# Kernel tuning notes

Measured on AMD Instinct MI355X. Metric: run time of the kernel, lower is better.

Reference implementation:

```python
import jax, jax.numpy as jnp
import numpy as np

N = 100000          # nodes
E = 1600000         # edges (avg degree 16)
D = 128             # prototype feature dim
C = 100             # num classes
NUM_LAYERS = 3      # propagation layers


def setup_inputs() -> dict:
    key = jax.random.key(0)
    k1, k2, k3, k4 = jax.random.split(key, 4)
    train_mask = jax.random.randint(k1, (N,), 0, 2) > 0                # bool [N]
    labels_all = jax.random.randint(k2, (N,), 0, C)                    # int   [N]
    edge_index = jax.random.randint(k3, (2, E), 0, N)                  # int   [2,E]
    global_protos = jax.random.normal(k4, (C, D), dtype=jnp.float32)   # [C,D]
    alpha = jnp.float32(0.5)                                           # learnable scalar
    return dict(train_mask=train_mask, global_protos=global_protos,
                labels_all=labels_all, edge_index=edge_index, alpha=alpha)


def _label_propagate(y0, edge_index, alpha):
    # symmetric GCN normalization D^-1/2 A D^-1/2 (no self loops), as in PyG LabelPropagation
    src, dst = edge_index[0], edge_index[1]
    deg = jax.ops.segment_sum(jnp.ones((E,), y0.dtype), dst, num_segments=N)
    deg_inv_sqrt = jnp.where(deg > 0, jax.lax.rsqrt(jnp.maximum(deg, 1.0)), 0.0)
    norm = deg_inv_sqrt[src] * deg_inv_sqrt[dst]                       # [E]
    res = (1.0 - alpha) * y0                                           # residual term
    out = y0
    for _ in range(NUM_LAYERS):
        msgs = out[src] * norm[:, None]                                # gather [E,D]
        agg = jax.ops.segment_sum(msgs, dst, num_segments=N)           # scatter-add [N,D]
        out = jnp.clip(alpha * agg + res, 0.0, 1.0)                    # post_step clamp
    return out


def reference(train_mask, global_protos, labels_all, edge_index, alpha):
    # proto_rep[train_mask] = global_protos[labels_all[train_mask]], zeros elsewhere
    y0 = jnp.where(train_mask[:, None], global_protos[labels_all], 0.0)  # [N,D]
    return _label_propagate(y0, edge_index, alpha)
```

## Files before the change

kernel.cpp:

```cpp
#include <hip/hip_runtime.h>
#include <stdint.h>

#define N_NODES 100000
#define N_EDGES 1600000
#define CAP     64
#define NBINS   1563
#define BINCAP  256
#define NSETS   8
#define CSTRIDE 16


__global__ void bin_kernel(const int* __restrict__ src, const int* __restrict__ dst,
                           int* __restrict__ cursor, unsigned int* __restrict__ bins) {
    int i = blockIdx.x * 256 + threadIdx.x;
    int set = blockIdx.x & 7;
    if (i < N_EDGES) {
        int s = src[i];
        int d = dst[i];
        int cid = set * NBINS + (d >> 6);
        int pos = atomicAdd(&cursor[cid * CSTRIDE], 1);
        if (pos < BINCAP)
            bins[(size_t)cid * BINCAP + pos] =
                (unsigned)s | ((unsigned)(d & 63) << 17);
    }
}


__global__ __launch_bounds__(256) void csr_kernel(
    const unsigned int* __restrict__ bins, const int* __restrict__ cursor,
    int* __restrict__ cnt, int* __restrict__ csr, float* __restrict__ dis,
    const int* __restrict__ mask, const int* __restrict__ labels,
    int* __restrict__ c0) {
    __shared__ int lc[64];
    int bin = blockIdx.x;
    int t = threadIdx.x;
    if (t < 64) lc[t] = 0;
    __syncthreads();
    int base = bin << 6;
    for (int set = 0; set < NSETS; ++set) {
        int cid = set * NBINS + bin;
        int m = cursor[cid * CSTRIDE];
        if (m > BINCAP) m = BINCAP;
        const unsigned int* seg = bins + (size_t)cid * BINCAP;
        for (int i = t; i < m; i += 256) {
            unsigned int v = seg[i];
            int dl = (int)(v >> 17);
            int pos = atomicAdd(&lc[dl], 1);
            if (pos < CAP) csr[(size_t)(base + dl) * CAP + pos] = (int)(v & 0x1FFFF);
        }
    }
    __syncthreads();
    if (t < 64) {
        int n = base + t;
        if (n < N_NODES) {
            int d = lc[t];
            cnt[n] = d;
            dis[n] = (d > 0) ? rsqrtf((float)d) : 0.0f;
            c0[n] = mask[n] ? labels[n] : -1;
        }
    }
}

template <int MODE>
__global__ __launch_bounds__(256) void prop_kernel(
    const uchar4* __restrict__ cur, void* __restrict__ out,
    const int* __restrict__ cnt, const int* __restrict__ csr,
    const float* __restrict__ dis, const int* __restrict__ c0,
    const float* __restrict__ protos, const float* __restrict__ alpha_p) {
    int wave = threadIdx.x >> 6;
    int lane = threadIdx.x & 63;
    int half = lane >> 5;
    int sub  = lane & 31;
    int base_lane = half << 5;
    int n = blockIdx.x * 8 + wave * 2 + half;

    float alpha = *alpha_p;
    int m = cnt[n];
    if (m > CAP) m = CAP;
    float dn = dis[n];
    const int* bucket = csr + (size_t)n * CAP;
    const float4* proto4 = (const float4*)protos;
    const float inv255 = 1.0f / 255.0f;

    int sl = 0;  float wl = 0.f;  int cl = -1;
    if (sub < m) {
        sl = bucket[sub];
        wl = dis[sl] * dn;
        if (MODE == 0) cl = c0[sl];
    }
    int sl2 = 0; float wl2 = 0.f; int cl2 = -1;
    if (m > 32 && 32 + sub < m) {
        sl2 = bucket[32 + sub];
        wl2 = dis[sl2] * dn;
        if (MODE == 0) cl2 = c0[sl2];
    }
    int m_other = __shfl(m, lane ^ 32);
    int mmax = m > m_other ? m : m_other;

    float a0 = 0.f, a1 = 0.f, a2 = 0.f, a3 = 0.f;

    if (MODE == 0) {
        for (int j = 0; j < mmax; j += 4) {
            float w[4]; float4 v[4];
            bool lo = j < 32;
#pragma unroll
            for (int k = 0; k < 4; ++k) {
                int e = j + k;
                float ww; int c;
                if (lo) { ww = __shfl(wl,  base_lane + e);      c = __shfl(cl,  base_lane + e); }
                else    { ww = __shfl(wl2, base_lane + e - 32); c = __shfl(cl2, base_lane + e - 32); }
                w[k] = ww;
                v[k] = (c >= 0) ? proto4[c * 32 + sub] : make_float4(0.f, 0.f, 0.f, 0.f);
            }
#pragma unroll
            for (int k = 0; k < 4; ++k) {
                a0 = fmaf(w[k], v[k].x, a0);
                a1 = fmaf(w[k], v[k].y, a1);
                a2 = fmaf(w[k], v[k].z, a2);
                a3 = fmaf(w[k], v[k].w, a3);
            }
        }
    } else {
        uchar4 u[8];  float w[8];
        uchar4 u2[8]; float w2[8];
#pragma unroll
        for (int k = 0; k < 8; ++k) {
            float ww = __shfl(wl, base_lane + k);
            int   s  = __shfl(sl, base_lane + k);
            w[k] = ww;
            u[k] = cur[(size_t)s * 32 + sub];
        }
        for (int j = 0; j < mmax; j += 8) {
            int jn = j + 8;
            if (jn < mmax) {
                bool lo = jn < 32;
#pragma unroll
                for (int k = 0; k < 8; ++k) {
                    int e = jn + k;
                    float ww; int s;
                    if (lo) { ww = __shfl(wl,  base_lane + e);      s = __shfl(sl,  base_lane + e); }
                    else    { ww = __shfl(wl2, base_lane + e - 32); s = __shfl(sl2, base_lane + e - 32); }
                    w2[k] = ww;
                    u2[k] = cur[(size_t)s * 32 + sub];
                }
            }
#pragma unroll
            for (int k = 0; k < 8; ++k) {
                float ws = w[k] * inv255;
                a0 = fmaf(ws, (float)u[k].x, a0);
                a1 = fmaf(ws, (float)u[k].y, a1);
                a2 = fmaf(ws, (float)u[k].z, a2);
                a3 = fmaf(ws, (float)u[k].w, a3);
            }
#pragma unroll
            for (int k = 0; k < 8; ++k) { u[k] = u2[k]; w[k] = w2[k]; }
        }
    }

    float y0x = 0.f, y0y = 0.f, y0z = 0.f, y0w = 0.f;
    int cn = c0[n];
    if (cn >= 0) {
        float4 p = proto4[cn * 32 + sub];
        y0x = p.x; y0y = p.y; y0z = p.z; y0w = p.w;
    }
    float ra = 1.f - alpha;
    float o0 = fminf(fmaxf(fmaf(alpha, a0, ra * y0x), 0.f), 1.f);
    float o1 = fminf(fmaxf(fmaf(alpha, a1, ra * y0y), 0.f), 1.f);
    float o2 = fminf(fmaxf(fmaf(alpha, a2, ra * y0z), 0.f), 1.f);
    float o3 = fminf(fmaxf(fmaf(alpha, a3, ra * y0w), 0.f), 1.f);

    if (MODE == 2) {
        ((float4*)out)[(size_t)n * 32 + sub] = make_float4(o0, o1, o2, o3);
    } else {
        uchar4 q;
        q.x = (unsigned char)(o0 * 255.f + 0.5f);
        q.y = (unsigned char)(o1 * 255.f + 0.5f);
        q.z = (unsigned char)(o2 * 255.f + 0.5f);
        q.w = (unsigned char)(o3 * 255.f + 0.5f);
        ((uchar4*)out)[(size_t)n * 32 + sub] = q;
    }
}


extern "C" void kernel_launch(void* const* d_in, const int* in_sizes, int n_in,
                              void* d_out, int out_size, void* d_ws, size_t ws_size,
                              hipStream_t stream) {
    const int*   mask   = (const int*)d_in[0];
    const float* protos = (const float*)d_in[1];
    const int*   labels = (const int*)d_in[2];
    const int*   ei     = (const int*)d_in[3];
    const float* alpha  = (const float*)d_in[4];
    const int* src = ei;
    const int* dst = ei + N_EDGES;

    int*          cursor = (int*)d_ws;
    int*          cnt    = cursor + NSETS * NBINS * CSTRIDE;
    float*        dis    = (float*)(cnt + N_NODES);
    int*          c0     = (int*)(dis + N_NODES);
    int*          csr    = c0 + N_NODES;
    unsigned int* bins   = (unsigned int*)(csr + (size_t)N_NODES * CAP);
    uchar4*       bufA   = (uchar4*)(bins + (size_t)NSETS * NBINS * BINCAP);
    uchar4*       bufB   = bufA + (size_t)N_NODES * 32;

    hipMemsetAsync(cursor, 0, NSETS * NBINS * CSTRIDE * sizeof(int), stream);

    bin_kernel<<<(N_EDGES + 255) / 256, 256, 0, stream>>>(src, dst, cursor, bins);
    csr_kernel<<<NBINS, 256, 0, stream>>>(bins, cursor, cnt, csr, dis,
                                          mask, labels, c0);

    int pgrid = N_NODES / 8;
    prop_kernel<0><<<pgrid, 256, 0, stream>>>(nullptr, bufA, cnt, csr, dis, c0,
                                              protos, alpha);
    prop_kernel<1><<<pgrid, 256, 0, stream>>>(bufA, bufB, cnt, csr, dis, c0,
                                              protos, alpha);
    prop_kernel<2><<<pgrid, 256, 0, stream>>>(bufB, d_out, cnt, csr, dis, c0,
                                              protos, alpha);
}
```

Measured before the change: 269.1 us.

## Split uint8 feature buffer into column chunks and gather per-chunk with edge-parallel lanes

Stores the quantized intermediate features as four 32-byte column chunks per node, each in its own plane, instead of one 128-byte row. The propagation kernel loops over chunks, and each group of 8 lanes handles a different edge, followed by a cross-lane reduction. The aim is for each chunk pass to touch a smaller working set (about 3.2 MB per plane) that fits in cache better, and to spread the random gathers across more edges at once. In exchange, every wave now loops four times and pays for extra shuffle reductions, and the per-edge gathers are narrower 32-byte segments.

```diff
diff --git a/kernel.cpp b/kernel.cpp
--- a/kernel.cpp
+++ b/kernel.cpp
@@ -8,6 +8,8 @@
 #define BINCAP  256
 #define NSETS   8
 #define CSTRIDE 16
+#define NCHUNK  4
+#define CH_BYTES ((size_t)N_NODES * 32)
 
 
 __global__ void bin_kernel(const int* __restrict__ src, const int* __restrict__ dst,
@@ -61,9 +63,75 @@
     }
 }
 
-template <int MODE>
-__global__ __launch_bounds__(256) void prop_kernel(
-    const uchar4* __restrict__ cur, void* __restrict__ out,
+
+__global__ __launch_bounds__(256) void prop0_kernel(
+    unsigned char* __restrict__ out, const int* __restrict__ cnt,
+    const int* __restrict__ csr, const float* __restrict__ dis,
+    const int* __restrict__ c0, const float* __restrict__ protos,
+    const float* __restrict__ alpha_p) {
+    int wave = threadIdx.x >> 6;
+    int lane = threadIdx.x & 63;
+    int half = lane >> 5;
+    int sub  = lane & 31;
+    int base_lane = half << 5;
+    int n = blockIdx.x * 8 + wave * 2 + half;
+
+    float alpha = *alpha_p;
+    int m = cnt[n];
+    if (m > CAP) m = CAP;
+    float dn = dis[n];
+    const int* bucket = csr + (size_t)n * CAP;
+    const float4* proto4 = (const float4*)protos;
+
+    int sl = 0;  float wl = 0.f;  int cl = -1;
+    if (sub < m)                { sl = bucket[sub];      wl = dis[sl] * dn;  cl = c0[sl]; }
+    int sl2 = 0; float wl2 = 0.f; int cl2 = -1;
+    if (m > 32 && 32 + sub < m) { sl2 = bucket[32 + sub]; wl2 = dis[sl2] * dn; cl2 = c0[sl2]; }
+    int m_other = __shfl(m, lane ^ 32);
+    int mmax = m > m_other ? m : m_other;
+
+    float a0 = 0.f, a1 = 0.f, a2 = 0.f, a3 = 0.f;
+    for (int j = 0; j < mmax; j += 4) {
+        bool lo = j < 32;
+#pragma unroll
+        for (int k = 0; k < 4; ++k) {
+            int e = j + k;
+            float ww; int c;
+            if (lo) { ww = __shfl(wl,  base_lane + e);      c = __shfl(cl,  base_lane + e); }
+            else    { ww = __shfl(wl2, base_lane + e - 32); c = __shfl(cl2, base_lane + e - 32); }
+            float4 v = (c >= 0) ? proto4[c * 32 + sub] : make_float4(0.f, 0.f, 0.f, 0.f);
+            a0 = fmaf(ww, v.x, a0);
+            a1 = fmaf(ww, v.y, a1);
+            a2 = fmaf(ww, v.z, a2);
+            a3 = fmaf(ww, v.w, a3);
+        }
+    }
+
+    float y0x = 0.f, y0y = 0.f, y0z = 0.f, y0w = 0.f;
+    int cn = c0[n];
+    if (cn >= 0) {
+        float4 p = proto4[cn * 32 + sub];
+        y0x = p.x; y0y = p.y; y0z = p.z; y0w = p.w;
+    }
+    float ra = 1.f - alpha;
+    float o0 = fminf(fmaxf(fmaf(alpha, a0, ra * y0x), 0.f), 1.f);
+    float o1 = fminf(fmaxf(fmaf(alpha, a1, ra * y0y), 0.f), 1.f);
+    float o2 = fminf(fmaxf(fmaf(alpha, a2, ra * y0z), 0.f), 1.f);
+    float o3 = fminf(fmaxf(fmaf(alpha, a3, ra * y0w), 0.f), 1.f);
+
+    uchar4 q;
+    q.x = (unsigned char)(o0 * 255.f + 0.5f);
+    q.y = (unsigned char)(o1 * 255.f + 0.5f);
+    q.z = (unsigned char)(o2 * 255.f + 0.5f);
+    q.w = (unsigned char)(o3 * 255.f + 0.5f);
+    uchar4* cb = (uchar4*)(out + (size_t)(sub >> 3) * CH_BYTES);
+    cb[(size_t)n * 8 + (sub & 7)] = q;
+}
+
+
+template <int LAST>
+__global__ __launch_bounds__(256) void propc_kernel(
+    const unsigned char* __restrict__ cur, void* __restrict__ out,
     const int* __restrict__ cnt, const int* __restrict__ csr,
     const float* __restrict__ dis, const int* __restrict__ c0,
     const float* __restrict__ protos, const float* __restrict__ alpha_p) {
@@ -72,6 +140,8 @@
     int half = lane >> 5;
     int sub  = lane & 31;
     int base_lane = half << 5;
+    int g = sub >> 3;
+    int q = sub & 7;
     int n = blockIdx.x * 8 + wave * 2 + half;
 
     float alpha = *alpha_p;
@@ -82,70 +152,47 @@
     const float4* proto4 = (const float4*)protos;
     const float inv255 = 1.0f / 255.0f;
 
-    int sl = 0;  float wl = 0.f;  int cl = -1;
-    if (sub < m) {
-        sl = bucket[sub];
-        wl = dis[sl] * dn;
-        if (MODE == 0) cl = c0[sl];
-    }
-    int sl2 = 0; float wl2 = 0.f; int cl2 = -1;
-    if (m > 32 && 32 + sub < m) {
-        sl2 = bucket[32 + sub];
-        wl2 = dis[sl2] * dn;
-        if (MODE == 0) cl2 = c0[sl2];
-    }
+    int sl = 0;  float wl = 0.f;
+    if (sub < m)                { sl = bucket[sub];       wl = dis[sl] * dn; }
+    int sl2 = 0; float wl2 = 0.f;
+    if (m > 32 && 32 + sub < m) { sl2 = bucket[32 + sub]; wl2 = dis[sl2] * dn; }
     int m_other = __shfl(m, lane ^ 32);
     int mmax = m > m_other ? m : m_other;
 
-    float a0 = 0.f, a1 = 0.f, a2 = 0.f, a3 = 0.f;
-
-    if (MODE == 0) {
-        for (int j = 0; j < mmax; j += 4) {
-            float w[4]; float4 v[4];
-            bool lo = j < 32;
-#pragma unroll
-            for (int k = 0; k < 4; ++k) {
-                int e = j + k;
-                float ww; int c;
-                if (lo) { ww = __shfl(wl,  base_lane + e);      c = __shfl(cl,  base_lane + e); }
-                else    { ww = __shfl(wl2, base_lane + e - 32); c = __shfl(cl2, base_lane + e - 32); }
-                w[k] = ww;
-                v[k] = (c >= 0) ? proto4[c * 32 + sub] : make_float4(0.f, 0.f, 0.f, 0.f);
-            }
-#pragma unroll
-            for (int k = 0; k < 4; ++k) {
-                a0 = fmaf(w[k], v[k].x, a0);
-                a1 = fmaf(w[k], v[k].y, a1);
-                a2 = fmaf(w[k], v[k].z, a2);
-                a3 = fmaf(w[k], v[k].w, a3);
-            }
-        }
-    } else {
-        uchar4 u[8];  float w[8];
-        uchar4 u2[8]; float w2[8];
-#pragma unroll
-        for (int k = 0; k < 8; ++k) {
-            float ww = __shfl(wl, base_lane + k);
-            int   s  = __shfl(sl, base_lane + k);
-            w[k] = ww;
-            u[k] = cur[(size_t)s * 32 + sub];
+    int cn = c0[n];
+    float ra = 1.f - alpha;
+
+    for (int c = 0; c < NCHUNK; ++c) {
+        const uchar4* cb = (const uchar4*)(cur + (size_t)c * CH_BYTES);
+        float a0 = 0.f, a1 = 0.f, a2 = 0.f, a3 = 0.f;
+
+        uchar4 u[2]; float w[2];
+        uchar4 u2[2]; float w2[2];
+        {
+            int e0 = g, e1 = 4 + g;
+            w[0] = __shfl(wl, base_lane + e0);
+            w[1] = __shfl(wl, base_lane + e1);
+            int s0 = __shfl(sl, base_lane + e0);
+            int s1 = __shfl(sl, base_lane + e1);
+            u[0] = cb[(size_t)s0 * 8 + q];
+            u[1] = cb[(size_t)s1 * 8 + q];
         }
         for (int j = 0; j < mmax; j += 8) {
             int jn = j + 8;
             if (jn < mmax) {
                 bool lo = jn < 32;
 #pragma unroll
-                for (int k = 0; k < 8; ++k) {
-                    int e = jn + k;
+                for (int k = 0; k < 2; ++k) {
+                    int e = jn + k * 4 + g;
                     float ww; int s;
                     if (lo) { ww = __shfl(wl,  base_lane + e);      s = __shfl(sl,  base_lane + e); }
                     else    { ww = __shfl(wl2, base_lane + e - 32); s = __shfl(sl2, base_lane + e - 32); }
                     w2[k] = ww;
-                    u2[k] = cur[(size_t)s * 32 + sub];
+                    u2[k] = cb[(size_t)s * 8 + q];
                 }
             }
 #pragma unroll
-            for (int k = 0; k < 8; ++k) {
+            for (int k = 0; k < 2; ++k) {
                 float ws = w[k] * inv255;
                 a0 = fmaf(ws, (float)u[k].x, a0);
                 a1 = fmaf(ws, (float)u[k].y, a1);
@@ -153,31 +200,38 @@
                 a3 = fmaf(ws, (float)u[k].w, a3);
             }
 #pragma unroll
-            for (int k = 0; k < 8; ++k) { u[k] = u2[k]; w[k] = w2[k]; }
-        }
-    }
-
-    float y0x = 0.f, y0y = 0.f, y0z = 0.f, y0w = 0.f;
-    int cn = c0[n];
-    if (cn >= 0) {
-        float4 p = proto4[cn * 32 + sub];
-        y0x = p.x; y0y = p.y; y0z = p.z; y0w = p.w;
-    }
-    float ra = 1.f - alpha;
-    float o0 = fminf(fmaxf(fmaf(alpha, a0, ra * y0x), 0.f), 1.f);
-    float o1 = fminf(fmaxf(fmaf(alpha, a1, ra * y0y), 0.f), 1.f);
-    float o2 = fminf(fmaxf(fmaf(alpha, a2, ra * y0z), 0.f), 1.f);
-    float o3 = fminf(fmaxf(fmaf(alpha, a3, ra * y0w), 0.f), 1.f);
-
-    if (MODE == 2) {
-        ((float4*)out)[(size_t)n * 32 + sub] = make_float4(o0, o1, o2, o3);
-    } else {
-        uchar4 q;
-        q.x = (unsigned char)(o0 * 255.f + 0.5f);
-        q.y = (unsigned char)(o1 * 255.f + 0.5f);
-        q.z = (unsigned char)(o2 * 255.f + 0.5f);
-        q.w = (unsigned char)(o3 * 255.f + 0.5f);
-        ((uchar4*)out)[(size_t)n * 32 + sub] = q;
+            for (int k = 0; k < 2; ++k) { u[k] = u2[k]; w[k] = w2[k]; }
+        }
+
+        a0 += __shfl_xor(a0, 8);  a0 += __shfl_xor(a0, 16);
+        a1 += __shfl_xor(a1, 8);  a1 += __shfl_xor(a1, 16);
+        a2 += __shfl_xor(a2, 8);  a2 += __shfl_xor(a2, 16);
+        a3 += __shfl_xor(a3, 8);  a3 += __shfl_xor(a3, 16);
+
+        float y0x = 0.f, y0y = 0.f, y0z = 0.f, y0w = 0.f;
+        if (cn >= 0) {
+            float4 p = proto4[cn * 32 + c * 8 + q];
+            y0x = p.x; y0y = p.y; y0z = p.z; y0w = p.w;
+        }
+        float o0 = fminf(fmaxf(fmaf(alpha, a0, ra * y0x), 0.f), 1.f);
+        float o1 = fminf(fmaxf(fmaf(alpha, a1, ra * y0y), 0.f), 1.f);
+        float o2 = fminf(fmaxf(fmaf(alpha, a2, ra * y0z), 0.f), 1.f);
+        float o3 = fminf(fmaxf(fmaf(alpha, a3, ra * y0w), 0.f), 1.f);
+
+        if (g == 0) {
+            if (LAST) {
+                ((float4*)out)[(size_t)n * 32 + c * 8 + q] =
+                    make_float4(o0, o1, o2, o3);
+            } else {
+                uchar4 qq;
+                qq.x = (unsigned char)(o0 * 255.f + 0.5f);
+                qq.y = (unsigned char)(o1 * 255.f + 0.5f);
+                qq.z = (unsigned char)(o2 * 255.f + 0.5f);
+                qq.w = (unsigned char)(o3 * 255.f + 0.5f);
+                ((uchar4*)((unsigned char*)out + (size_t)c * CH_BYTES))
+                    [(size_t)n * 8 + q] = qq;
+            }
+        }
     }
 }
 
@@ -193,14 +247,14 @@
     const int* src = ei;
     const int* dst = ei + N_EDGES;
 
-    int*          cursor = (int*)d_ws;
-    int*          cnt    = cursor + NSETS * NBINS * CSTRIDE;
-    float*        dis    = (float*)(cnt + N_NODES);
-    int*          c0     = (int*)(dis + N_NODES);
-    int*          csr    = c0 + N_NODES;
-    unsigned int* bins   = (unsigned int*)(csr + (size_t)N_NODES * CAP);
-    uchar4*       bufA   = (uchar4*)(bins + (size_t)NSETS * NBINS * BINCAP);
-    uchar4*       bufB   = bufA + (size_t)N_NODES * 32;
+    int*           cursor = (int*)d_ws;
+    int*           cnt    = cursor + NSETS * NBINS * CSTRIDE;
+    float*         dis    = (float*)(cnt + N_NODES);
+    int*           c0     = (int*)(dis + N_NODES);
+    int*           csr    = c0 + N_NODES;
+    unsigned int*  bins   = (unsigned int*)(csr + (size_t)N_NODES * CAP);
+    unsigned char* bufA   = (unsigned char*)(bins + (size_t)NSETS * NBINS * BINCAP);
+    unsigned char* bufB   = bufA + NCHUNK * CH_BYTES;
 
     hipMemsetAsync(cursor, 0, NSETS * NBINS * CSTRIDE * sizeof(int), stream);
 
@@ -209,10 +263,9 @@
                                           mask, labels, c0);
 
     int pgrid = N_NODES / 8;
-    prop_kernel<0><<<pgrid, 256, 0, stream>>>(nullptr, bufA, cnt, csr, dis, c0,
-                                              protos, alpha);
-    prop_kernel<1><<<pgrid, 256, 0, stream>>>(bufA, bufB, cnt, csr, dis, c0,
-                                              protos, alpha);
-    prop_kernel<2><<<pgrid, 256, 0, stream>>>(bufB, d_out, cnt, csr, dis, c0,
-                                              protos, alpha);
-}
+    prop0_kernel<<<pgrid, 256, 0, stream>>>(bufA, cnt, csr, dis, c0, protos, alpha);
+    propc_kernel<0><<<pgrid, 256, 0, stream>>>(bufA, bufB, cnt, csr, dis, c0,
+                                               protos, alpha);
+    propc_kernel<1><<<pgrid, 256, 0, stream>>>(bufB, d_out, cnt, csr, dis, c0,
+                                               protos, alpha);
+}
```

After: 371.1 us. 1.38x slower.
